# Kernel tuning notes

Measured on AMD Instinct MI355X. Metric: run time of the kernel, lower is better.

Reference implementation:

```python
import jax, jax.numpy as jnp
import numpy as np

N_NODES = 100000


def gcn_conv(x, edge_index, W, b, n_nodes):
    # PyG GCNConv: x' = D^{-1/2} (A + I) D^{-1/2} (x W) + b
    src, dst = edge_index[0], edge_index[1]
    h = x @ W  # linear transform first (in_ch >= out_ch path in PyG)
    # degree with self-loops, computed on target nodes
    deg = jax.ops.segment_sum(jnp.ones_like(dst, dtype=h.dtype), dst,
                              num_segments=n_nodes) + 1.0
    dinv = jax.lax.rsqrt(deg)  # deg >= 1 due to self-loops
    # edge messages: norm_e * h[src]
    norm_e = dinv[src] * dinv[dst]  # [E]
    msg = h[src] * norm_e[:, None]  # [E, out]
    agg = jax.ops.segment_sum(msg, dst, num_segments=n_nodes)
    # self-loop contribution: dinv[i]^2 * h[i]
    out = agg + h * (dinv * dinv)[:, None] + b
    return out


def setup_inputs() -> dict:
    key = jax.random.key(0)
    k1, k2, k3, k4 = jax.random.split(key, 4)
    N, E, F, H, C = N_NODES, 1600000, 128, 64, 32
    x = jax.random.normal(k1, (N, F), dtype=jnp.float32)
    edge_index = jax.random.randint(k2, (2, E), 0, N, dtype=jnp.int64)
    # glorot-style init
    W1 = jax.random.normal(k3, (F, H), dtype=jnp.float32) * (1.0 / np.sqrt(F))
    W2 = jax.random.normal(k4, (H, C), dtype=jnp.float32) * (1.0 / np.sqrt(H))
    b1 = jnp.zeros((H,), dtype=jnp.float32)
    b2 = jnp.zeros((C,), dtype=jnp.float32)
    return {"x": x, "edge_index": edge_index, "W1": W1, "b1": b1,
            "W2": W2, "b2": b2}


def reference(x, edge_index, W1, b1, W2, b2):
    n = x.shape[0]
    h = gcn_conv(x, edge_index, W1, b1, n)
    h = jax.nn.relu(h)
    # dropout is identity in eval mode (reference baseline)
    out = gcn_conv(h, edge_index, W2, b2, n)
    return out
```

## Files before the change

kernel.cpp:

```cpp
#include <hip/hip_runtime.h>
#include <hip/hip_fp16.h>

#define B_HIST 512
#define SHIFT  9


__global__ __launch_bounds__(256) void p1_hist(const int* __restrict__ dst,
                                               int* __restrict__ histT, int E) {
  __shared__ int h[256];
  const int t = threadIdx.x;
  h[t] = 0;
  __syncthreads();
  const int epb = (E + B_HIST - 1) / B_HIST;
  const int beg = blockIdx.x * epb;
  const int end = min(beg + epb, E);
  for (int e = beg + t; e < end; e += 256)
    atomicAdd(&h[dst[e] >> SHIFT], 1);
  __syncthreads();
  histT[t * B_HIST + blockIdx.x] = h[t];
}

__global__ __launch_bounds__(256) void p2a_colscan(int* __restrict__ histT,
                                                   int* __restrict__ bsum) {
  __shared__ int sdata[256];
  const int bin = blockIdx.x, t = threadIdx.x;
  const int i0 = bin * B_HIST + 2 * t;
  int c0 = histT[i0], c1 = histT[i0 + 1];
  int s = c0 + c1;
  sdata[t] = s;
  __syncthreads();
  for (int off = 1; off < 256; off <<= 1) {
    int x = 0;
    if (t >= off) x = sdata[t - off];
    __syncthreads();
    if (t >= off) sdata[t] += x;
    __syncthreads();
  }
  int excl = sdata[t] - s;
  histT[i0] = excl;
  histT[i0 + 1] = excl + c0;
  if (t == 255) bsum[bin] = sdata[255];
}

__global__ __launch_bounds__(256) void p2b_scan(const int* __restrict__ bsum,
                                                int* __restrict__ colstart) {
  __shared__ int sdata[256];
  const int t = threadIdx.x;
  int v = bsum[t];
  sdata[t] = v;
  __syncthreads();
  for (int off = 1; off < 256; off <<= 1) {
    int x = 0;
    if (t >= off) x = sdata[t - off];
    __syncthreads();
    if (t >= off) sdata[t] += x;
    __syncthreads();
  }
  colstart[t] = sdata[t] - v;
  if (t == 255) colstart[256] = sdata[255];
}

__global__ __launch_bounds__(256) void p3_scatter(const int* __restrict__ src,
                                                  const int* __restrict__ dst,
                                                  const int* __restrict__ histT,
                                                  const int* __restrict__ colstart,
                                                  int* __restrict__ pbuf, int E) {
  __shared__ int cur[256];
  const int t = threadIdx.x;
  cur[t] = colstart[t] + histT[t * B_HIST + blockIdx.x];
  __syncthreads();
  const int epb = (E + B_HIST - 1) / B_HIST;
  const int beg = blockIdx.x * epb;
  const int end = min(beg + epb, E);
  for (int e = beg + t; e < end; e += 256) {
    int d = dst[e];
    int s = src[e];
    int pos = atomicAdd(&cur[d >> SHIFT], 1);
    pbuf[pos] = ((d & 511) << 17) | s;
  }
}

__global__ __launch_bounds__(256) void p4_fine(const int* __restrict__ pbuf,
                                               const int* __restrict__ colstart,
                                               int* __restrict__ rowptr,
                                               float* __restrict__ dinv,
                                               int* __restrict__ ssrc, int N, int NB) {
  __shared__ int cnt[512];
  __shared__ int sdata[256];
  __shared__ int cur[512];
  const int b = blockIdx.x, t = threadIdx.x;
  const int base = colstart[b], endp = colstart[b + 1];
  cnt[2 * t] = 0; cnt[2 * t + 1] = 0;
  __syncthreads();
  for (int i = base + t; i < endp; i += 256)
    atomicAdd(&cnt[pbuf[i] >> 17], 1);
  __syncthreads();
  int c0 = cnt[2 * t], c1 = cnt[2 * t + 1];
  int s = c0 + c1;
  sdata[t] = s;
  __syncthreads();
  for (int off = 1; off < 256; off <<= 1) {
    int x = 0;
    if (t >= off) x = sdata[t - off];
    __syncthreads();
    if (t >= off) sdata[t] += x;
    __syncthreads();
  }
  int excl = sdata[t] - s;
  int e0 = base + excl, e1 = base + excl + c0;
  cur[2 * t] = e0;
  cur[2 * t + 1] = e1;
  int node0 = (b << SHIFT) + 2 * t;
  if (node0 < N) {
    rowptr[node0] = e0;
    dinv[node0] = rsqrtf((float)c0 + 1.0f);
  }
  if (node0 + 1 < N) {
    rowptr[node0 + 1] = e1;
    dinv[node0 + 1] = rsqrtf((float)c1 + 1.0f);
  }
  if (b == NB - 1 && t == 0) rowptr[N] = endp;
  __syncthreads();
  for (int i = base + t; i < endp; i += 256) {
    int p = pbuf[i];
    int pos = atomicAdd(&cur[p >> 17], 1);
    ssrc[pos] = p & 0x1FFFF;
  }
}


template <int ROWS, int COLS, int K>
__global__ __launch_bounds__(256) void gemmk4_kernel(const float* __restrict__ X,
                                                     const float* __restrict__ W,
                                                     const float* __restrict__ dinv,
                                                     __half* __restrict__ O, int N) {
  __shared__ float xs[ROWS][K + 4];
  __shared__ float ws[K][COLS];
  const int t = threadIdx.x;
  const int row0 = blockIdx.x * ROWS;

  constexpr int WV = K * COLS / 4;
  for (int i = t; i < WV; i += 256) {
    float4 v = reinterpret_cast<const float4*>(W)[i];
    int base = i * 4;
    int k = base / COLS, c = base % COLS;
    ws[k][c] = v.x; ws[k][c + 1] = v.y; ws[k][c + 2] = v.z; ws[k][c + 3] = v.w;
  }
  constexpr int XV = ROWS * K / 4;
  for (int i = t; i < XV; i += 256) {
    int base = i * 4;
    int r = base / K, k = base % K;
    int row = row0 + r;
    float4 v = make_float4(0.f, 0.f, 0.f, 0.f);
    if (row < N) v = reinterpret_cast<const float4*>(X + (size_t)row * K)[k >> 2];
    *reinterpret_cast<float4*>(&xs[r][k]) = v;
  }
  __syncthreads();

  constexpr int TC = COLS / 4;
  const int tc = t % TC, tr = t / TC;
  const int c0 = tc * 4, r0 = tr * 4;
  float acc[4][4] = {{0.f}};

  for (int k = 0; k < K; k += 4) {
    float4 a[4], b[4];
#pragma unroll
    for (int i = 0; i < 4; ++i)
      a[i] = *reinterpret_cast<const float4*>(&xs[r0 + i][k]);
#pragma unroll
    for (int j = 0; j < 4; ++j)
      b[j] = *reinterpret_cast<const float4*>(&ws[k + j][c0]);
#pragma unroll
    for (int i = 0; i < 4; ++i) {
      acc[i][0] = fmaf(a[i].x, b[0].x, acc[i][0]);
      acc[i][1] = fmaf(a[i].x, b[0].y, acc[i][1]);
      acc[i][2] = fmaf(a[i].x, b[0].z, acc[i][2]);
      acc[i][3] = fmaf(a[i].x, b[0].w, acc[i][3]);
      acc[i][0] = fmaf(a[i].y, b[1].x, acc[i][0]);
      acc[i][1] = fmaf(a[i].y, b[1].y, acc[i][1]);
      acc[i][2] = fmaf(a[i].y, b[1].z, acc[i][2]);
      acc[i][3] = fmaf(a[i].y, b[1].w, acc[i][3]);
      acc[i][0] = fmaf(a[i].z, b[2].x, acc[i][0]);
      acc[i][1] = fmaf(a[i].z, b[2].y, acc[i][1]);
      acc[i][2] = fmaf(a[i].z, b[2].z, acc[i][2]);
      acc[i][3] = fmaf(a[i].z, b[2].w, acc[i][3]);
      acc[i][0] = fmaf(a[i].w, b[3].x, acc[i][0]);
      acc[i][1] = fmaf(a[i].w, b[3].y, acc[i][1]);
      acc[i][2] = fmaf(a[i].w, b[3].z, acc[i][2]);
      acc[i][3] = fmaf(a[i].w, b[3].w, acc[i][3]);
    }
  }

#pragma unroll
  for (int i = 0; i < 4; ++i) {
    int row = row0 + r0 + i;
    if (row < N) {
      float di = dinv[row];
      __half2 p01 = __floats2half2_rn(acc[i][0] * di, acc[i][1] * di);
      __half2 p23 = __floats2half2_rn(acc[i][2] * di, acc[i][3] * di);
      union { __half2 h2[2]; uint2 u; } cvt;
      cvt.h2[0] = p01; cvt.h2[1] = p23;
      *reinterpret_cast<uint2*>(O + (size_t)row * COLS + c0) = cvt.u;
    }
  }
}


template <int ROWS, int COLS, int K>
__global__ __launch_bounds__(256) void gemm_kernel(const float* __restrict__ X,
                                                   const float* __restrict__ W,
                                                   const float* __restrict__ dinv,
                                                   __half* __restrict__ O, int N) {
  __shared__ float xs[ROWS][K + 4];
  __shared__ float ws[K][COLS];
  const int t = threadIdx.x;
  const int row0 = blockIdx.x * ROWS;

  constexpr int WV = K * COLS / 4;
  for (int i = t; i < WV; i += 256) {
    float4 v = reinterpret_cast<const float4*>(W)[i];
    int base = i * 4;
    int k = base / COLS, c = base % COLS;
    ws[k][c] = v.x; ws[k][c + 1] = v.y; ws[k][c + 2] = v.z; ws[k][c + 3] = v.w;
  }
  constexpr int XV = ROWS * K / 4;
  for (int i = t; i < XV; i += 256) {
    int base = i * 4;
    int r = base / K, k = base % K;
    int row = row0 + r;
    float4 v = make_float4(0.f, 0.f, 0.f, 0.f);
    if (row < N) v = reinterpret_cast<const float4*>(X + (size_t)row * K)[k >> 2];
    *reinterpret_cast<float4*>(&xs[r][k]) = v;
  }
  __syncthreads();

  constexpr int TC = COLS / 4;
  const int tc = t % TC, tr = t / TC;
  const int c0 = tc * 4, r0 = tr * 4;
  float acc[4][4] = {{0.f}};

#pragma unroll 8
  for (int k = 0; k < K; ++k) {
    float a0 = xs[r0 + 0][k];
    float a1 = xs[r0 + 1][k];
    float a2 = xs[r0 + 2][k];
    float a3 = xs[r0 + 3][k];
    float4 b = *reinterpret_cast<const float4*>(&ws[k][c0]);
    acc[0][0] = fmaf(a0, b.x, acc[0][0]); acc[0][1] = fmaf(a0, b.y, acc[0][1]);
    acc[0][2] = fmaf(a0, b.z, acc[0][2]); acc[0][3] = fmaf(a0, b.w, acc[0][3]);
    acc[1][0] = fmaf(a1, b.x, acc[1][0]); acc[1][1] = fmaf(a1, b.y, acc[1][1]);
    acc[1][2] = fmaf(a1, b.z, acc[1][2]); acc[1][3] = fmaf(a1, b.w, acc[1][3]);
    acc[2][0] = fmaf(a2, b.x, acc[2][0]); acc[2][1] = fmaf(a2, b.y, acc[2][1]);
    acc[2][2] = fmaf(a2, b.z, acc[2][2]); acc[2][3] = fmaf(a2, b.w, acc[2][3]);
    acc[3][0] = fmaf(a3, b.x, acc[3][0]); acc[3][1] = fmaf(a3, b.y, acc[3][1]);
    acc[3][2] = fmaf(a3, b.z, acc[3][2]); acc[3][3] = fmaf(a3, b.w, acc[3][3]);
  }

#pragma unroll
  for (int i = 0; i < 4; ++i) {
    int row = row0 + r0 + i;
    if (row < N) {
      float di = dinv[row];
      __half2 p01 = __floats2half2_rn(acc[i][0] * di, acc[i][1] * di);
      __half2 p23 = __floats2half2_rn(acc[i][2] * di, acc[i][3] * di);
      union { __half2 h2[2]; uint2 u; } cvt;
      cvt.h2[0] = p01; cvt.h2[1] = p23;
      *reinterpret_cast<uint2*>(O + (size_t)row * COLS + c0) = cvt.u;
    }
  }
}


__global__ __launch_bounds__(256) void gather64_kernel(const int* __restrict__ rowptr,
                                                       const int* __restrict__ ssrc,
                                                       const float* __restrict__ dinv,
                                                       const uint2* __restrict__ g,
                                                       const float4* __restrict__ bias,
                                                       float4* __restrict__ outb, int N) {
  int node = (blockIdx.x * 256 + threadIdx.x) >> 4;
  int col = threadIdx.x & 15;
  if (node >= N) return;
  int beg = rowptr[node], end = rowptr[node + 1];
  float4 a0 = {0.f, 0.f, 0.f, 0.f}, a1 = a0;
  for (int i = beg; i < end; i += 8) {
    int cnt = end - i;
    uint2 v[8];
#pragma unroll
    for (int u = 0; u < 8; ++u) {
      if (u < cnt) {
        int s = ssrc[i + u];
        v[u] = g[(size_t)s * 16 + col];
      }
    }
#pragma unroll
    for (int u = 0; u < 8; ++u) {
      if (u < cnt) {
        float2 f0 = __half22float2(*(__half2*)&v[u].x);
        float2 f1 = __half22float2(*(__half2*)&v[u].y);
        if (u & 1) { a1.x += f0.x; a1.y += f0.y; a1.z += f1.x; a1.w += f1.y; }
        else       { a0.x += f0.x; a0.y += f0.y; a0.z += f1.x; a0.w += f1.y; }
      }
    }
  }
  uint2 vs = g[(size_t)node * 16 + col];
  float2 g01 = __half22float2(*(__half2*)&vs.x);
  float2 g23 = __half22float2(*(__half2*)&vs.y);
  float di = dinv[node];
  float4 bb = bias[col];
  float4 o;
  o.x = fmaxf(fmaf(di, (a0.x + a1.x) + g01.x, bb.x), 0.f);
  o.y = fmaxf(fmaf(di, (a0.y + a1.y) + g01.y, bb.y), 0.f);
  o.z = fmaxf(fmaf(di, (a0.z + a1.z) + g23.x, bb.z), 0.f);
  o.w = fmaxf(fmaf(di, (a0.w + a1.w) + g23.y, bb.w), 0.f);
  outb[(size_t)node * 16 + col] = o;
}

__global__ __launch_bounds__(256) void gather32_kernel(const int* __restrict__ rowptr,
                                                       const int* __restrict__ ssrc,
                                                       const float* __restrict__ dinv,
                                                       const uint2* __restrict__ g,
                                                       const float4* __restrict__ bias,
                                                       float4* __restrict__ outb, int N) {
  int node = (blockIdx.x * 256 + threadIdx.x) >> 3;
  int col = threadIdx.x & 7;
  if (node >= N) return;
  int beg = rowptr[node], end = rowptr[node + 1];
  float4 a0 = {0.f, 0.f, 0.f, 0.f}, a1 = a0;
  for (int i = beg; i < end; i += 8) {
    int cnt = end - i;
    uint2 v[8];
#pragma unroll
    for (int u = 0; u < 8; ++u) {
      if (u < cnt) {
        int s = ssrc[i + u];
        v[u] = g[(size_t)s * 8 + col];
      }
    }
#pragma unroll
    for (int u = 0; u < 8; ++u) {
      if (u < cnt) {
        float2 f0 = __half22float2(*(__half2*)&v[u].x);
        float2 f1 = __half22float2(*(__half2*)&v[u].y);
        if (u & 1) { a1.x += f0.x; a1.y += f0.y; a1.z += f1.x; a1.w += f1.y; }
        else       { a0.x += f0.x; a0.y += f0.y; a0.z += f1.x; a0.w += f1.y; }
      }
    }
  }
  uint2 vs = g[(size_t)node * 8 + col];
  float2 g01 = __half22float2(*(__half2*)&vs.x);
  float2 g23 = __half22float2(*(__half2*)&vs.y);
  float di = dinv[node];
  float4 bb = bias[col];
  float4 o;
  o.x = fmaf(di, (a0.x + a1.x) + g01.x, bb.x);
  o.y = fmaf(di, (a0.y + a1.y) + g01.y, bb.y);
  o.z = fmaf(di, (a0.z + a1.z) + g23.x, bb.z);
  o.w = fmaf(di, (a0.w + a1.w) + g23.y, bb.w);
  outb[(size_t)node * 8 + col] = o;
}


extern "C" void kernel_launch(void* const* d_in, const int* in_sizes, int n_in,
                              void* d_out, int out_size, void* d_ws, size_t ws_size,
                              hipStream_t stream) {
  const float* x  = (const float*)d_in[0];
  const int*   ei = (const int*)d_in[1];
  const float* W1 = (const float*)d_in[2];
  const float* b1 = (const float*)d_in[3];
  const float* W2 = (const float*)d_in[4];
  const float* b2 = (const float*)d_in[5];
  float* out = (float*)d_out;

  const int H = in_sizes[3];
  const int F = in_sizes[2] / H;
  const int N = in_sizes[0] / F;
  const int E = in_sizes[1] / 2;
  const int* src = ei;
  const int* dst = ei + E;
  const int NB = (N + 511) >> SHIFT;

  char* w = (char*)d_ws;
  auto alloc = [&](size_t bytes) { char* p = w; w += (bytes + 255) & ~(size_t)255; return p; };
  int*    histT    = (int*)alloc((size_t)256 * B_HIST * 4);
  int*    bsum     = (int*)alloc(256 * 4);
  int*    colstart = (int*)alloc(257 * 4);
  int*    pbuf     = (int*)alloc((size_t)E * 4);
  int*    ssrc     = (int*)alloc((size_t)E * 4);
  int*    rowptr   = (int*)alloc((size_t)(N + 1) * 4);
  float*  dinv     = (float*)alloc((size_t)N * 4);
  __half* g1       = (__half*)alloc((size_t)N * 64 * 2);
  float*  buf1     = (float*)alloc((size_t)N * 64 * 4);
  __half* g2       = (__half*)alloc((size_t)N * 32 * 2);

  p1_hist<<<B_HIST, 256, 0, stream>>>(dst, histT, E);
  p2a_colscan<<<256, 256, 0, stream>>>(histT, bsum);
  p2b_scan<<<1, 256, 0, stream>>>(bsum, colstart);
  p3_scatter<<<B_HIST, 256, 0, stream>>>(src, dst, histT, colstart, pbuf, E);
  p4_fine<<<NB, 256, 0, stream>>>(pbuf, colstart, rowptr, dinv, ssrc, N, NB);

  gemmk4_kernel<64, 64, 128><<<(N + 63) / 64, 256, 0, stream>>>(x, W1, dinv, g1, N);
  gather64_kernel<<<(N * 16 + 255) / 256, 256, 0, stream>>>(rowptr, ssrc, dinv,
      (const uint2*)g1, (const float4*)b1, (float4*)buf1, N);

  gemm_kernel<128, 32, 64><<<(N + 127) / 128, 256, 0, stream>>>(buf1, W2, dinv, g2, N);
  gather32_kernel<<<(N * 8 + 255) / 256, 256, 0, stream>>>(rowptr, ssrc, dinv,
      (const uint2*)g2, (const float4*)b2, (float4*)out, N);
}
```

Before: 172.0 us.

## Replace FP32 FMA GEMMs with fp16 MFMA matrix-core GEMM kernel

Both dense transforms now run through one templated kernel. It converts X and W tiles to fp16 in shared memory, using an XOR swizzle on X, and computes with the 16x16x32 f16 MFMA instruction instead of scalar FP32 FMAs. The aim is to cut the compute and LDS cost of the two GEMMs. The inputs are now rounded to fp16 before the multiply, which lowers precision. The output stores also become scalar half writes with less coalescing.

```diff
diff --git a/kernel.cpp b/kernel.cpp
--- a/kernel.cpp
+++ b/kernel.cpp
@@ -3,6 +3,9 @@
 
 #define B_HIST 512
 #define SHIFT  9
+
+typedef _Float16 f16x8 __attribute__((ext_vector_type(8)));
+typedef float f32x4 __attribute__((ext_vector_type(4)));
 
 
 __global__ __launch_bounds__(256) void p1_hist(const int* __restrict__ dst,
@@ -129,143 +132,79 @@
 }
 
 
-template <int ROWS, int COLS, int K>
-__global__ __launch_bounds__(256) void gemmk4_kernel(const float* __restrict__ X,
-                                                     const float* __restrict__ W,
-                                                     const float* __restrict__ dinv,
-                                                     __half* __restrict__ O, int N) {
-  __shared__ float xs[ROWS][K + 4];
-  __shared__ float ws[K][COLS];
+template <int COLS, int K>
+__global__ __launch_bounds__(256) void mfma_gemm(const float* __restrict__ X,
+                                                 const float* __restrict__ W,
+                                                 const float* __restrict__ dinv,
+                                                 __half* __restrict__ O, int N) {
+  constexpr int NKK = K / 32;
+  constexpr int NCT = COLS / 16;
+  constexpr int RCH = K / 8;
+  constexpr int SWM = RCH - 1;
+  __shared__ _Float16 xs[64 * K];
+  __shared__ _Float16 wb[K * COLS];
   const int t = threadIdx.x;
-  const int row0 = blockIdx.x * ROWS;
-
-  constexpr int WV = K * COLS / 4;
-  for (int i = t; i < WV; i += 256) {
-    float4 v = reinterpret_cast<const float4*>(W)[i];
-    int base = i * 4;
-    int k = base / COLS, c = base % COLS;
-    ws[k][c] = v.x; ws[k][c + 1] = v.y; ws[k][c + 2] = v.z; ws[k][c + 3] = v.w;
-  }
-  constexpr int XV = ROWS * K / 4;
-  for (int i = t; i < XV; i += 256) {
-    int base = i * 4;
-    int r = base / K, k = base % K;
-    int row = row0 + r;
-    float4 v = make_float4(0.f, 0.f, 0.f, 0.f);
-    if (row < N) v = reinterpret_cast<const float4*>(X + (size_t)row * K)[k >> 2];
-    *reinterpret_cast<float4*>(&xs[r][k]) = v;
-  }
-  __syncthreads();
-
-  constexpr int TC = COLS / 4;
-  const int tc = t % TC, tr = t / TC;
-  const int c0 = tc * 4, r0 = tr * 4;
-  float acc[4][4] = {{0.f}};
-
-  for (int k = 0; k < K; k += 4) {
-    float4 a[4], b[4];
-#pragma unroll
-    for (int i = 0; i < 4; ++i)
-      a[i] = *reinterpret_cast<const float4*>(&xs[r0 + i][k]);
-#pragma unroll
-    for (int j = 0; j < 4; ++j)
-      b[j] = *reinterpret_cast<const float4*>(&ws[k + j][c0]);
-#pragma unroll
-    for (int i = 0; i < 4; ++i) {
-      acc[i][0] = fmaf(a[i].x, b[0].x, acc[i][0]);
-      acc[i][1] = fmaf(a[i].x, b[0].y, acc[i][1]);
-      acc[i][2] = fmaf(a[i].x, b[0].z, acc[i][2]);
-      acc[i][3] = fmaf(a[i].x, b[0].w, acc[i][3]);
-      acc[i][0] = fmaf(a[i].y, b[1].x, acc[i][0]);
-      acc[i][1] = fmaf(a[i].y, b[1].y, acc[i][1]);
-      acc[i][2] = fmaf(a[i].y, b[1].z, acc[i][2]);
-      acc[i][3] = fmaf(a[i].y, b[1].w, acc[i][3]);
-      acc[i][0] = fmaf(a[i].z, b[2].x, acc[i][0]);
-      acc[i][1] = fmaf(a[i].z, b[2].y, acc[i][1]);
-      acc[i][2] = fmaf(a[i].z, b[2].z, acc[i][2]);
-      acc[i][3] = fmaf(a[i].z, b[2].w, acc[i][3]);
-      acc[i][0] = fmaf(a[i].w, b[3].x, acc[i][0]);
-      acc[i][1] = fmaf(a[i].w, b[3].y, acc[i][1]);
-      acc[i][2] = fmaf(a[i].w, b[3].z, acc[i][2]);
-      acc[i][3] = fmaf(a[i].w, b[3].w, acc[i][3]);
-    }
-  }
-
-#pragma unroll
-  for (int i = 0; i < 4; ++i) {
-    int row = row0 + r0 + i;
+  const int row0 = blockIdx.x * 64;
+
+  for (int task = t; task < NKK * 4 * COLS; task += 256) {
+    int col = task % COLS;
+    int kq = task / COLS;
+    _Float16 tmp[8];
+#pragma unroll
+    for (int j = 0; j < 8; ++j)
+      tmp[j] = (_Float16)W[(kq * 8 + j) * COLS + col];
+    *reinterpret_cast<f16x8*>(&wb[task * 8]) = *reinterpret_cast<const f16x8*>(tmp);
+  }
+  for (int task = t; task < 64 * RCH; task += 256) {
+    int row = task / RCH, c = task % RCH;
+    int grow = row0 + row;
+    float4 v0 = make_float4(0.f, 0.f, 0.f, 0.f), v1 = v0;
+    if (grow < N) {
+      const float4* xr = reinterpret_cast<const float4*>(X + (size_t)grow * K);
+      v0 = xr[c * 2];
+      v1 = xr[c * 2 + 1];
+    }
+    _Float16 tmp[8] = {(_Float16)v0.x, (_Float16)v0.y, (_Float16)v0.z, (_Float16)v0.w,
+                       (_Float16)v1.x, (_Float16)v1.y, (_Float16)v1.z, (_Float16)v1.w};
+    int sc = c ^ (row & SWM);
+    *reinterpret_cast<f16x8*>(&xs[row * K + sc * 8]) = *reinterpret_cast<const f16x8*>(tmp);
+  }
+  __syncthreads();
+
+  const int wave = t >> 6, lane = t & 63;
+  const int q = lane >> 4, c = lane & 15;
+  const int wrow = wave * 16;
+
+  f16x8 bfrag[NKK][NCT];
+#pragma unroll
+  for (int kk = 0; kk < NKK; ++kk)
+#pragma unroll
+    for (int ct = 0; ct < NCT; ++ct)
+      bfrag[kk][ct] = *reinterpret_cast<const f16x8*>(
+          &wb[(size_t)((kk * 4 + q) * COLS + ct * 16 + c) * 8]);
+
+  f32x4 acc[NCT];
+#pragma unroll
+  for (int ct = 0; ct < NCT; ++ct) acc[ct] = {0.f, 0.f, 0.f, 0.f};
+
+#pragma unroll
+  for (int kk = 0; kk < NKK; ++kk) {
+    int row = wrow + c;
+    int cc = (kk * 4 + q) ^ (row & SWM);
+    f16x8 afrag = *reinterpret_cast<const f16x8*>(&xs[row * K + cc * 8]);
+#pragma unroll
+    for (int ct = 0; ct < NCT; ++ct)
+      acc[ct] = __builtin_amdgcn_mfma_f32_16x16x32_f16(afrag, bfrag[kk][ct], acc[ct], 0, 0, 0);
+  }
+
+#pragma unroll
+  for (int r = 0; r < 4; ++r) {
+    int row = row0 + wrow + q * 4 + r;
     if (row < N) {
       float di = dinv[row];
-      __half2 p01 = __floats2half2_rn(acc[i][0] * di, acc[i][1] * di);
-      __half2 p23 = __floats2half2_rn(acc[i][2] * di, acc[i][3] * di);
-      union { __half2 h2[2]; uint2 u; } cvt;
-      cvt.h2[0] = p01; cvt.h2[1] = p23;
-      *reinterpret_cast<uint2*>(O + (size_t)row * COLS + c0) = cvt.u;
-    }
-  }
-}
-
-
-template <int ROWS, int COLS, int K>
-__global__ __launch_bounds__(256) void gemm_kernel(const float* __restrict__ X,
-                                                   const float* __restrict__ W,
-                                                   const float* __restrict__ dinv,
-                                                   __half* __restrict__ O, int N) {
-  __shared__ float xs[ROWS][K + 4];
-  __shared__ float ws[K][COLS];
-  const int t = threadIdx.x;
-  const int row0 = blockIdx.x * ROWS;
-
-  constexpr int WV = K * COLS / 4;
-  for (int i = t; i < WV; i += 256) {
-    float4 v = reinterpret_cast<const float4*>(W)[i];
-    int base = i * 4;
-    int k = base / COLS, c = base % COLS;
-    ws[k][c] = v.x; ws[k][c + 1] = v.y; ws[k][c + 2] = v.z; ws[k][c + 3] = v.w;
-  }
-  constexpr int XV = ROWS * K / 4;
-  for (int i = t; i < XV; i += 256) {
-    int base = i * 4;
-    int r = base / K, k = base % K;
-    int row = row0 + r;
-    float4 v = make_float4(0.f, 0.f, 0.f, 0.f);
-    if (row < N) v = reinterpret_cast<const float4*>(X + (size_t)row * K)[k >> 2];
-    *reinterpret_cast<float4*>(&xs[r][k]) = v;
-  }
-  __syncthreads();
-
-  constexpr int TC = COLS / 4;
-  const int tc = t % TC, tr = t / TC;
-  const int c0 = tc * 4, r0 = tr * 4;
-  float acc[4][4] = {{0.f}};
-
-#pragma unroll 8
-  for (int k = 0; k < K; ++k) {
-    float a0 = xs[r0 + 0][k];
-    float a1 = xs[r0 + 1][k];
-    float a2 = xs[r0 + 2][k];
-    float a3 = xs[r0 + 3][k];
-    float4 b = *reinterpret_cast<const float4*>(&ws[k][c0]);
-    acc[0][0] = fmaf(a0, b.x, acc[0][0]); acc[0][1] = fmaf(a0, b.y, acc[0][1]);
-    acc[0][2] = fmaf(a0, b.z, acc[0][2]); acc[0][3] = fmaf(a0, b.w, acc[0][3]);
-    acc[1][0] = fmaf(a1, b.x, acc[1][0]); acc[1][1] = fmaf(a1, b.y, acc[1][1]);
-    acc[1][2] = fmaf(a1, b.z, acc[1][2]); acc[1][3] = fmaf(a1, b.w, acc[1][3]);
-    acc[2][0] = fmaf(a2, b.x, acc[2][0]); acc[2][1] = fmaf(a2, b.y, acc[2][1]);
-    acc[2][2] = fmaf(a2, b.z, acc[2][2]); acc[2][3] = fmaf(a2, b.w, acc[2][3]);
-    acc[3][0] = fmaf(a3, b.x, acc[3][0]); acc[3][1] = fmaf(a3, b.y, acc[3][1]);
-    acc[3][2] = fmaf(a3, b.z, acc[3][2]); acc[3][3] = fmaf(a3, b.w, acc[3][3]);
-  }
-
-#pragma unroll
-  for (int i = 0; i < 4; ++i) {
-    int row = row0 + r0 + i;
-    if (row < N) {
-      float di = dinv[row];
-      __half2 p01 = __floats2half2_rn(acc[i][0] * di, acc[i][1] * di);
-      __half2 p23 = __floats2half2_rn(acc[i][2] * di, acc[i][3] * di);
-      union { __half2 h2[2]; uint2 u; } cvt;
-      cvt.h2[0] = p01; cvt.h2[1] = p23;
-      *reinterpret_cast<uint2*>(O + (size_t)row * COLS + c0) = cvt.u;
+#pragma unroll
+      for (int ct = 0; ct < NCT; ++ct)
+        O[(size_t)row * COLS + ct * 16 + c] = __float2half(acc[ct][r] * di);
     }
   }
 }
@@ -398,11 +337,11 @@
   p3_scatter<<<B_HIST, 256, 0, stream>>>(src, dst, histT, colstart, pbuf, E);
   p4_fine<<<NB, 256, 0, stream>>>(pbuf, colstart, rowptr, dinv, ssrc, N, NB);
 
-  gemmk4_kernel<64, 64, 128><<<(N + 63) / 64, 256, 0, stream>>>(x, W1, dinv, g1, N);
+  mfma_gemm<64, 128><<<(N + 63) / 64, 256, 0, stream>>>(x, W1, dinv, g1, N);
   gather64_kernel<<<(N * 16 + 255) / 256, 256, 0, stream>>>(rowptr, ssrc, dinv,
       (const uint2*)g1, (const float4*)b1, (float4*)buf1, N);
 
-  gemm_kernel<128, 32, 64><<<(N + 127) / 128, 256, 0, stream>>>(buf1, W2, dinv, g2, N);
+  mfma_gemm<32, 64><<<(N + 63) / 64, 256, 0, stream>>>(buf1, W2, dinv, g2, N);
   gather32_kernel<<<(N * 8 + 255) / 256, 256, 0, stream>>>(rowptr, ssrc, dinv,
       (const uint2*)g2, (const float4*)b2, (float4*)out, N);
 }
```

After: 144.8 us. 1.19x faster.
